# Optimization experiments

Hardware: AMD Instinct MI355X
Metric: run time of the kernel (lower is better)

The kernel has to match this reference:

```python
import jax, jax.numpy as jnp
import numpy as np

N = 50000
E = 800000
IN_DIM, HID, OUT = 128, 64, 64
SLOPE = 0.2  # PyG GATConv default negative_slope


def gat_conv(x, W, a_src, a_dst, b, src, dst):
    """Single-head PyG GATConv, add_self_loops=False."""
    h = x @ W                                  # [N, F]
    alpha_s = h @ a_src                        # [N]
    alpha_d = h @ a_dst                        # [N]
    e = jax.nn.leaky_relu(alpha_s[src] + alpha_d[dst], SLOPE)   # [E]
    # segment softmax over incoming edges of each destination node
    m = jax.ops.segment_max(e, dst, num_segments=N)             # [N]
    w = jnp.exp(e - m[dst])                                     # [E]
    z = jax.ops.segment_sum(w, dst, num_segments=N)             # [N]
    alpha = w / z[dst]                                          # [E]
    out = jax.ops.segment_sum(h[src] * alpha[:, None], dst, num_segments=N)
    return out + b


def setup_inputs() -> dict:
    key = jax.random.key(0)
    ks = jax.random.split(key, 12)
    x = jax.random.normal(ks[0], (N, IN_DIM), dtype=jnp.float32)
    edge_index = jax.random.randint(ks[1], (2, E), 0, N, dtype=jnp.int64)
    s1 = 1.0 / np.sqrt(IN_DIM)
    s2 = 1.0 / np.sqrt(HID)
    return {
        "x": x,
        "edge_index": edge_index,
        "W1": jax.random.normal(ks[2], (IN_DIM, HID), dtype=jnp.float32) * s1,
        "att_src1": jax.random.normal(ks[3], (HID,), dtype=jnp.float32) * s2,
        "att_dst1": jax.random.normal(ks[4], (HID,), dtype=jnp.float32) * s2,
        "b1": jnp.zeros((HID,), dtype=jnp.float32),
        "W2": jax.random.normal(ks[5], (HID, OUT), dtype=jnp.float32) * s2,
        "att_src2": jax.random.normal(ks[6], (OUT,), dtype=jnp.float32) / np.sqrt(OUT),
        "att_dst2": jax.random.normal(ks[7], (OUT,), dtype=jnp.float32) / np.sqrt(OUT),
        "b2": jnp.zeros((OUT,), dtype=jnp.float32),
    }


def reference(x, edge_index, W1, att_src1, att_dst1, b1, W2, att_src2, att_dst2, b2):
    src, dst = edge_index[0], edge_index[1]
    h = gat_conv(x, W1, att_src1, att_dst1, b1, src, dst)
    h = jax.nn.relu(h)
    # dropout is identity in eval mode
    h = gat_conv(h, W2, att_src2, att_dst2, b2, src, dst)
    # F.normalize(p=2, dim=-1): divide by max(norm, eps)
    norm = jnp.linalg.norm(h, axis=-1, keepdims=True)
    return h / jnp.maximum(norm, 1e-12)
```

## Files before the change

### kernel.cpp

```cpp
#include <hip/hip_runtime.h>
#include <hip/hip_fp16.h>
#include <math.h>

#define NNODES 50000
#define NEDGES 800000
#define NBUCK 256
#define EPB 4096
#define NBLK1 ((NEDGES + EPB - 1) / EPB)
#define SCANL (NBUCK * NBLK1)
#define SCANB ((SCANL + 1023) / 1024)


__global__ __launch_bounds__(256) void k_bcount(const int* __restrict__ dst,
                                                int* __restrict__ bcnt) {
    __shared__ int h[NBUCK];
    int t = threadIdx.x, b = blockIdx.x;
    h[t] = 0;
    __syncthreads();
    int beg = b * EPB, end = min(beg + EPB, NEDGES);
    for (int e = beg + t; e < end; e += 256) atomicAdd(&h[dst[e] >> 8], 1);
    __syncthreads();
    bcnt[t * NBLK1 + b] = h[t];
}

__global__ void k_scan_block(const int* __restrict__ in, int* __restrict__ out,
                             int* __restrict__ partial, int n) {
    __shared__ int tmp[1024];
    int t = threadIdx.x;
    int i = blockIdx.x * 1024 + t;
    int v = (i < n) ? in[i] : 0;
    tmp[t] = v;
    __syncthreads();
    for (int off = 1; off < 1024; off <<= 1) {
        int u = (t >= off) ? tmp[t - off] : 0;
        __syncthreads();
        tmp[t] += u;
        __syncthreads();
    }
    if (i < n) out[i] = tmp[t] - v;
    if (t == 1023) partial[blockIdx.x] = tmp[t];
}

__device__ __forceinline__ void scan_partials(const int* __restrict__ partial, int* sp) {
    int t = threadIdx.x;
    if (t < 64) {
        int v = (t < SCANB) ? partial[t] : 0;
        int incl = v;
        #pragma unroll
        for (int off = 1; off < 64; off <<= 1) {
            int u = __shfl_up(incl, off, 64);
            if (t >= off) incl += u;
        }
        if (t < SCANB) sp[t] = incl - v;
    }
    __syncthreads();
}

__global__ __launch_bounds__(256) void k_bscatter(const int* __restrict__ src,
                                                  const int* __restrict__ dst,
                                                  const int* __restrict__ boffs,
                                                  const int* __restrict__ partial,
                                                  int2* __restrict__ ep) {
    __shared__ int cur[NBUCK];
    __shared__ int sp[SCANB];
    int t = threadIdx.x, b = blockIdx.x;
    scan_partials(partial, sp);
    int idx = t * NBLK1 + b;
    cur[t] = boffs[idx] + sp[idx >> 10];
    __syncthreads();
    int beg = b * EPB, end = min(beg + EPB, NEDGES);
    for (int e = beg + t; e < end; e += 256) {
        int d = dst[e];
        int pos = atomicAdd(&cur[d >> 8], 1);
        ep[pos] = make_int2(d, src[e]);
    }
}

__global__ __launch_bounds__(512) void k_fine(const int2* __restrict__ ep,
                                              const int* __restrict__ boffs,
                                              const int* __restrict__ partial,
                                              int* __restrict__ offs,
                                              int* __restrict__ esrc) {
    __shared__ int h[NBUCK];
    __shared__ int cur[NBUCK];
    __shared__ int sp[SCANB];
    int t = threadIdx.x, buck = blockIdx.x;
    scan_partials(partial, sp);
    int bi = buck * NBLK1;
    int base = boffs[bi] + sp[bi >> 10];
    int endp;
    if (buck == NBUCK - 1) endp = NEDGES;
    else {
        int ei2 = (buck + 1) * NBLK1;
        endp = boffs[ei2] + sp[ei2 >> 10];
    }
    if (t < NBUCK) h[t] = 0;
    __syncthreads();
    for (int i = base + t; i < endp; i += 512) atomicAdd(&h[ep[i].x & 255], 1);
    __syncthreads();
    int v = (t < NBUCK) ? h[t] : 0;
    for (int off = 1; off < 256; off <<= 1) {
        int u = (t >= off && t < NBUCK) ? h[t - off] : 0;
        __syncthreads();
        if (t < NBUCK) h[t] += u;
        __syncthreads();
    }
    if (t < NBUCK) {
        int excl = h[t] - v;
        int node = buck * 256 + t;
        if (node <= NNODES) offs[node] = base + excl;
        cur[t] = base + excl;
    }
    __syncthreads();
    for (int i = base + t; i < endp; i += 512) {
        int2 p = ep[i];
        int pos = atomicAdd(&cur[p.x & 255], 1);
        esrc[pos] = p.y;
    }
}


__device__ __forceinline__ void fma4(float4& a, float s, const float4& w) {
    a.x = fmaf(s, w.x, a.x);
    a.y = fmaf(s, w.y, a.y);
    a.z = fmaf(s, w.z, a.z);
    a.w = fmaf(s, w.w, a.w);
}

template<int K, int XH>
__global__ __launch_bounds__(256, 2) void k_gemm_att(
    const void* __restrict__ Xv, const float* __restrict__ W,
    const float* __restrict__ a_src, const float* __restrict__ a_dst,
    __half* __restrict__ H, float* __restrict__ AS, float* __restrict__ AD, int N)
{
    constexpr int KF = K / 4;
    constexpr int KFS = (K == 128) ? 5 : 4;
    __shared__ float Xs[64 * K];
    __shared__ float Ws[K * 64];
    int t = threadIdx.x;
    int n0 = blockIdx.x * 64;

    const float4* W4 = (const float4*)W;
    #pragma unroll
    for (int f = t; f < K * 16; f += 256)
        ((float4*)Ws)[f] = W4[f];
    #pragma unroll
    for (int f = t; f < 64 * KF; f += 256) {
        int r = f >> KFS, k4 = f & (KF - 1);
        float4 v = {0.f, 0.f, 0.f, 0.f};
        if (n0 + r < N) {
            if (XH) {
                union { uint2 u; __half2 h2[2]; } c;
                c.u = ((const uint2*)Xv)[(size_t)(n0 + r) * KF + k4];
                float2 lo = __half22float2(c.h2[0]);
                float2 hi = __half22float2(c.h2[1]);
                v = make_float4(lo.x, lo.y, hi.x, hi.y);
            } else {
                v = ((const float4*)Xv)[(size_t)(n0 + r) * KF + k4];
            }
        }
        ((float4*)&Xs[r * K])[k4 ^ ((r >> 2) & 3)] = v;
    }
    __syncthreads();

    int tr = t >> 4, tc = t & 15;
    int xi = tr & 3;
    const float4* xr0 = (const float4*)&Xs[(tr * 4 + 0) * K];
    const float4* xr1 = (const float4*)&Xs[(tr * 4 + 1) * K];
    const float4* xr2 = (const float4*)&Xs[(tr * 4 + 2) * K];
    const float4* xr3 = (const float4*)&Xs[(tr * 4 + 3) * K];
    float4 acc0 = {}, acc1 = {}, acc2 = {}, acc3 = {};

    #pragma unroll 2
    for (int k4 = 0; k4 < KF; ++k4) {
        int sl = k4 ^ xi;
        float4 x0 = xr0[sl], x1 = xr1[sl], x2 = xr2[sl], x3 = xr3[sl];
        float4 w0 = *(const float4*)&Ws[(k4 * 4 + 0) * 64 + tc * 4];
        float4 w1 = *(const float4*)&Ws[(k4 * 4 + 1) * 64 + tc * 4];
        float4 w2 = *(const float4*)&Ws[(k4 * 4 + 2) * 64 + tc * 4];
        float4 w3 = *(const float4*)&Ws[(k4 * 4 + 3) * 64 + tc * 4];
        fma4(acc0, x0.x, w0); fma4(acc0, x0.y, w1); fma4(acc0, x0.z, w2); fma4(acc0, x0.w, w3);
        fma4(acc1, x1.x, w0); fma4(acc1, x1.y, w1); fma4(acc1, x1.z, w2); fma4(acc1, x1.w, w3);
        fma4(acc2, x2.x, w0); fma4(acc2, x2.y, w1); fma4(acc2, x2.z, w2); fma4(acc2, x2.w, w3);
        fma4(acc3, x3.x, w0); fma4(acc3, x3.y, w1); fma4(acc3, x3.z, w2); fma4(acc3, x3.w, w3);
    }

    float4 asv = *(const float4*)&a_src[tc * 4];
    float4 adv = *(const float4*)&a_dst[tc * 4];
    float4 accs[4] = {acc0, acc1, acc2, acc3};
    #pragma unroll
    for (int i = 0; i < 4; ++i) {
        int row = n0 + tr * 4 + i;
        if (row < N) {
            float4 a = accs[i];
            float s1 = a.x * asv.x + a.y * asv.y + a.z * asv.z + a.w * asv.w;
            float s2 = a.x * adv.x + a.y * adv.y + a.z * adv.z + a.w * adv.w;
            #pragma unroll
            for (int o = 1; o < 16; o <<= 1) {
                s1 += __shfl_xor(s1, o, 64);
                s2 += __shfl_xor(s2, o, 64);
            }
            union { __half2 h2[2]; uint2 u; } pk;
            pk.h2[0] = __floats2half2_rn(a.x, a.y);
            pk.h2[1] = __floats2half2_rn(a.z, a.w);
            *(uint2*)&H[(size_t)row * 64 + tc * 4] = pk.u;
            if (tc == 0) { AS[row] = s1; AD[row] = s2; }
        }
    }
}

template<int RELU, int NORM, int OUTH>
__global__ __launch_bounds__(256) void k_agg(
    const int* __restrict__ esrc, const int* __restrict__ offs,
    const __half* __restrict__ H, const float* __restrict__ AS,
    const float* __restrict__ AD, const float* __restrict__ bias,
    void* __restrict__ outv, int N)
{
    __shared__ int2 sm[4][64];
    int gid = blockIdx.x * blockDim.x + threadIdx.x;
    int w = gid >> 6;
    int lane = gid & 63;
    int wid = threadIdx.x >> 6;
    int n0 = 2 * w;
    if (n0 >= N) return;
    int half = lane >> 5, fp = lane & 31;
    int nh = n0 + half;
    bool valid = nh < N;
    int beg = valid ? offs[nh] : 0;
    int end = valid ? offs[nh + 1] : 0;
    int deg = end - beg;
    int degO = __shfl_xor(deg, 32, 64);
    int dm = max(deg, degO);
    float2 bp = ((const float2*)bias)[fp];

    if (dm <= 32) {
        float add = valid ? AD[nh] : 0.f;
        int s = 0;
        float logit = -3.0e38f;
        if (fp < deg) {
            s = esrc[beg + fp];
            float l0 = AS[s] + add;
            logit = (l0 > 0.f) ? l0 : 0.2f * l0;
        }
        float m = logit;
        #pragma unroll
        for (int o = 16; o > 0; o >>= 1) m = fmaxf(m, __shfl_xor(m, o, 64));
        float wg = (fp < deg) ? __expf(logit - m) : 0.f;
        float z = wg;
        #pragma unroll
        for (int o = 16; o > 0; o >>= 1) z += __shfl_xor(z, o, 64);
        sm[wid][lane] = make_int2(s, __float_as_int(wg));

        const __half2* H2 = (const __half2*)H;
        float2 a0 = {0.f, 0.f}, a1 = {0.f, 0.f};
        int base = half * 32;
        int k = 0;
        for (; k + 1 < dm; k += 2) {
            int4 v = *(const int4*)&sm[wid][base + k];
            float2 h0 = __half22float2(H2[(size_t)v.x * 32 + fp]);
            float2 h1 = __half22float2(H2[(size_t)v.z * 32 + fp]);
            float w0 = __int_as_float(v.y), w1 = __int_as_float(v.w);
            a0.x = fmaf(w0, h0.x, a0.x); a0.y = fmaf(w0, h0.y, a0.y);
            a1.x = fmaf(w1, h1.x, a1.x); a1.y = fmaf(w1, h1.y, a1.y);
        }
        if (k < dm) {
            int2 v = sm[wid][base + k];
            float2 h0 = __half22float2(H2[(size_t)v.x * 32 + fp]);
            float w0 = __int_as_float(v.y);
            a0.x = fmaf(w0, h0.x, a0.x); a0.y = fmaf(w0, h0.y, a0.y);
        }
        float2 acc = {a0.x + a1.x, a0.y + a1.y};
        float rz = (deg > 0) ? (1.0f / z) : 0.f;
        float2 val2 = make_float2(fmaf(acc.x, rz, bp.x), fmaf(acc.y, rz, bp.y));
        if (RELU) { val2.x = fmaxf(val2.x, 0.f); val2.y = fmaxf(val2.y, 0.f); }
        if (NORM) {
            float ss = val2.x * val2.x + val2.y * val2.y;
            #pragma unroll
            for (int o = 16; o > 0; o >>= 1) ss += __shfl_xor(ss, o, 64);
            float inv = 1.0f / fmaxf(sqrtf(ss), 1e-12f);
            val2.x *= inv; val2.y *= inv;
        }
        if (valid) {
            if (OUTH) ((__half2*)outv)[(size_t)nh * 32 + fp] = __floats2half2_rn(val2.x, val2.y);
            else      ((float2*)outv)[(size_t)nh * 32 + fp] = val2;
        }
        return;
    }

    #pragma unroll 1
    for (int side = 0; side < 2; ++side) {
        int n = n0 + side;
        if (n >= N) break;
        int b2 = offs[n], e2 = offs[n + 1];
        int dg = e2 - b2;
        float add = AD[n];
        if (dg <= 64) {
            int s = 0;
            float logit = -3.0e38f;
            if (lane < dg) {
                s = esrc[b2 + lane];
                float l0 = AS[s] + add;
                logit = (l0 > 0.f) ? l0 : 0.2f * l0;
            }
            float m = logit;
            #pragma unroll
            for (int o = 32; o > 0; o >>= 1) m = fmaxf(m, __shfl_xor(m, o, 64));
            float wg = (lane < dg) ? __expf(logit - m) : 0.f;
            float z = wg;
            #pragma unroll
            for (int o = 32; o > 0; o >>= 1) z += __shfl_xor(z, o, 64);
            sm[wid][lane] = make_int2(s, __float_as_int(wg));
            const __half2* H2 = (const __half2*)H;
            float2 a0 = {0.f, 0.f};
            for (int k = half; k < dg; k += 2) {
                int2 v = sm[wid][k];
                float2 h0 = __half22float2(H2[(size_t)v.x * 32 + fp]);
                float w0 = __int_as_float(v.y);
                a0.x = fmaf(w0, h0.x, a0.x); a0.y = fmaf(w0, h0.y, a0.y);
            }
            a0.x += __shfl_xor(a0.x, 32, 64);
            a0.y += __shfl_xor(a0.y, 32, 64);
            float rz = (dg > 0) ? (1.0f / z) : 0.f;
            float2 val2 = make_float2(fmaf(a0.x, rz, bp.x), fmaf(a0.y, rz, bp.y));
            if (RELU) { val2.x = fmaxf(val2.x, 0.f); val2.y = fmaxf(val2.y, 0.f); }
            if (NORM) {
                float ss = val2.x * val2.x + val2.y * val2.y;
                #pragma unroll
                for (int o = 16; o > 0; o >>= 1) ss += __shfl_xor(ss, o, 64);
                float inv = 1.0f / fmaxf(sqrtf(ss), 1e-12f);
                val2.x *= inv; val2.y *= inv;
            }
            if (half == 0) {
                if (OUTH) ((__half2*)outv)[(size_t)n * 32 + fp] = __floats2half2_rn(val2.x, val2.y);
                else      ((float2*)outv)[(size_t)n * 32 + fp] = val2;
            }
        } else {
            float m = -3.0e38f, z = 0.f, acc = 0.f;
            for (int i = b2; i < e2; ++i) {
                int s = esrc[i];
                float l0 = AS[s] + add;
                l0 = (l0 > 0.f) ? l0 : 0.2f * l0;
                float mn = fmaxf(m, l0);
                float sc = __expf(m - mn);
                float wgt = __expf(l0 - mn);
                z = z * sc + wgt;
                acc = acc * sc + wgt * __half2float(H[(size_t)s * 64 + lane]);
                m = mn;
            }
            float val = acc / z + ((lane & 1) ? bp.y : bp.x);
            val = acc / z + bias[lane];
            if (RELU) val = fmaxf(val, 0.f);
            if (NORM) {
                float ss = val * val;
                #pragma unroll
                for (int o = 32; o > 0; o >>= 1) ss += __shfl_xor(ss, o, 64);
                val = val / fmaxf(sqrtf(ss), 1e-12f);
            }
            if (OUTH) ((__half*)outv)[(size_t)n * 64 + lane] = __float2half(val);
            else      ((float*)outv)[(size_t)n * 64 + lane] = val;
        }
    }
}


extern "C" void kernel_launch(void* const* d_in, const int* in_sizes, int n_in,
                              void* d_out, int out_size, void* d_ws, size_t ws_size,
                              hipStream_t stream) {
    const float* x   = (const float*)d_in[0];
    const int*   ei  = (const int*)d_in[1];
    const float* W1  = (const float*)d_in[2];
    const float* as1 = (const float*)d_in[3];
    const float* ad1 = (const float*)d_in[4];
    const float* b1  = (const float*)d_in[5];
    const float* W2  = (const float*)d_in[6];
    const float* as2 = (const float*)d_in[7];
    const float* ad2 = (const float*)d_in[8];
    const float* b2  = (const float*)d_in[9];
    const int* src = ei;
    const int* dst = ei + NEDGES;

    char* ws = (char*)d_ws;
    size_t off = 0;
    auto alloc = [&](size_t bytes) -> void* {
        void* p = ws + off;
        off = (off + bytes + 255) & ~(size_t)255;
        return p;
    };
    __half* H    = (__half*)alloc((size_t)NNODES * 64 * 2);
    __half* OUT1 = (__half*)alloc((size_t)NNODES * 64 * 2);
    float* AS    = (float*)alloc((size_t)NNODES * 4);
    float* AD    = (float*)alloc((size_t)NNODES * 4);
    int*   offs  = (int*)alloc((size_t)(NNODES + 1) * 4);
    int2*  ep    = (int2*)alloc((size_t)NEDGES * 8);
    int*   esrc  = (int*)alloc((size_t)NEDGES * 4);
    int*   bcnt  = (int*)alloc((size_t)SCANL * 4);
    int*   boffs = (int*)alloc((size_t)SCANL * 4);
    int*   part1 = (int*)alloc((size_t)SCANB * 4);

    k_bcount<<<NBLK1, 256, 0, stream>>>(dst, bcnt);
    k_scan_block<<<SCANB, 1024, 0, stream>>>(bcnt, boffs, part1, SCANL);
    k_bscatter<<<NBLK1, 256, 0, stream>>>(src, dst, boffs, part1, ep);
    k_fine<<<NBUCK, 512, 0, stream>>>(ep, boffs, part1, offs, esrc);

    int aggBlocks = (NNODES / 2 + 3) / 4;
    k_gemm_att<128, 0><<<(NNODES + 63) / 64, 256, 0, stream>>>(x, W1, as1, ad1, H, AS, AD, NNODES);
    k_agg<1, 0, 1><<<aggBlocks, 256, 0, stream>>>(esrc, offs, H, AS, AD, b1, OUT1, NNODES);

    k_gemm_att<64, 1><<<(NNODES + 63) / 64, 256, 0, stream>>>(OUT1, W2, as2, ad2, H, AS, AD, NNODES);
    k_agg<0, 1, 0><<<aggBlocks, 256, 0, stream>>>(esrc, offs, H, AS, AD, b2, d_out, NNODES);
}
```

Baseline: 120.9 us.

## Pack edge pairs into one int and stage fine sort in shared memory

The intermediate bucketed edge array now stores src<<8 | low dst byte in a single int instead of an int2, halving its write and read traffic. The fine per-bucket sort loads each bucket's edges into LDS once, builds the histogram and scatters into a shared sorted buffer, then writes esrc coalesced. This avoids rereading ep from global memory and the scattered global writes. A fallback keeps the global path when a bucket exceeds 8192 edges. The 64KB of LDS per block may reduce occupancy of k_fine, and packing assumes source ids fit in 24 bits.

New measurement: 118.2 us. 2.2% less time.

```diff
diff --git a/kernel.cpp b/kernel.cpp
--- a/kernel.cpp
+++ b/kernel.cpp
@@ -9,6 +9,7 @@
 #define NBLK1 ((NEDGES + EPB - 1) / EPB)
 #define SCANL (NBUCK * NBLK1)
 #define SCANB ((SCANL + 1023) / 1024)
+#define FCAP 8192
 
 
 __global__ __launch_bounds__(256) void k_bcount(const int* __restrict__ dst,
@@ -60,7 +61,7 @@
                                                   const int* __restrict__ dst,
                                                   const int* __restrict__ boffs,
                                                   const int* __restrict__ partial,
-                                                  int2* __restrict__ ep) {
+                                                  int* __restrict__ ep) {
     __shared__ int cur[NBUCK];
     __shared__ int sp[SCANB];
     int t = threadIdx.x, b = blockIdx.x;
@@ -72,11 +73,11 @@
     for (int e = beg + t; e < end; e += 256) {
         int d = dst[e];
         int pos = atomicAdd(&cur[d >> 8], 1);
-        ep[pos] = make_int2(d, src[e]);
-    }
-}
-
-__global__ __launch_bounds__(512) void k_fine(const int2* __restrict__ ep,
+        ep[pos] = (src[e] << 8) | (d & 255);
+    }
+}
+
+__global__ __launch_bounds__(512) void k_fine(const int* __restrict__ ep,
                                               const int* __restrict__ boffs,
                                               const int* __restrict__ partial,
                                               int* __restrict__ offs,
@@ -84,6 +85,8 @@
     __shared__ int h[NBUCK];
     __shared__ int cur[NBUCK];
     __shared__ int sp[SCANB];
+    __shared__ int stg[FCAP];
+    __shared__ int srt[FCAP];
     int t = threadIdx.x, buck = blockIdx.x;
     scan_partials(partial, sp);
     int bi = buck * NBLK1;
@@ -94,9 +97,18 @@
         int ei2 = (buck + 1) * NBLK1;
         endp = boffs[ei2] + sp[ei2 >> 10];
     }
+    int cnt = endp - base;
+    bool fits = (cnt <= FCAP);
+
     if (t < NBUCK) h[t] = 0;
     __syncthreads();
-    for (int i = base + t; i < endp; i += 512) atomicAdd(&h[ep[i].x & 255], 1);
+    if (fits) {
+        for (int j = t; j < cnt; j += 512) stg[j] = ep[base + j];
+        __syncthreads();
+        for (int j = t; j < cnt; j += 512) atomicAdd(&h[stg[j] & 255], 1);
+    } else {
+        for (int i = base + t; i < endp; i += 512) atomicAdd(&h[ep[i] & 255], 1);
+    }
     __syncthreads();
     int v = (t < NBUCK) ? h[t] : 0;
     for (int off = 1; off < 256; off <<= 1) {
@@ -109,13 +121,23 @@
         int excl = h[t] - v;
         int node = buck * 256 + t;
         if (node <= NNODES) offs[node] = base + excl;
-        cur[t] = base + excl;
-    }
-    __syncthreads();
-    for (int i = base + t; i < endp; i += 512) {
-        int2 p = ep[i];
-        int pos = atomicAdd(&cur[p.x & 255], 1);
-        esrc[pos] = p.y;
+        cur[t] = excl;
+    }
+    __syncthreads();
+    if (fits) {
+        for (int j = t; j < cnt; j += 512) {
+            int p = stg[j];
+            int pos = atomicAdd(&cur[p & 255], 1);
+            srt[pos] = p >> 8;
+        }
+        __syncthreads();
+        for (int j = t; j < cnt; j += 512) esrc[base + j] = srt[j];
+    } else {
+        for (int i = base + t; i < endp; i += 512) {
+            int p = ep[i];
+            int pos = atomicAdd(&cur[p & 255], 1);
+            esrc[base + pos] = p >> 8;
+        }
     }
 }
 
@@ -347,8 +369,7 @@
                 acc = acc * sc + wgt * __half2float(H[(size_t)s * 64 + lane]);
                 m = mn;
             }
-            float val = acc / z + ((lane & 1) ? bp.y : bp.x);
-            val = acc / z + bias[lane];
+            float val = acc / z + bias[lane];
             if (RELU) val = fmaxf(val, 0.f);
             if (NORM) {
                 float ss = val * val;
@@ -391,7 +412,7 @@
     float* AS    = (float*)alloc((size_t)NNODES * 4);
     float* AD    = (float*)alloc((size_t)NNODES * 4);
     int*   offs  = (int*)alloc((size_t)(NNODES + 1) * 4);
-    int2*  ep    = (int2*)alloc((size_t)NEDGES * 8);
+    int*   ep    = (int*)alloc((size_t)NEDGES * 4);
     int*   esrc  = (int*)alloc((size_t)NEDGES * 4);
     int*   bcnt  = (int*)alloc((size_t)SCANL * 4);
     int*   boffs = (int*)alloc((size_t)SCANL * 4);
```
